# Performance work log

Hardware: AMD Instinct MI355X
Metric: run time of the kernel (lower is better)

The kernel has to match this reference:

```python
import jax, jax.numpy as jnp
import numpy as np

N_VAR = 524288   # code.n
DV = 3           # regular variable-node degree
DC = 6           # regular check-node degree
N_CHK = N_VAR * DV // DC
T = 10           # max_iterations


def setup_inputs() -> dict:
    key = jax.random.key(0)
    k1, k2, k3 = jax.random.split(key, 3)
    rng = np.random.default_rng(0)
    # Regular (3,6) Tanner graph via random socket permutation (edge list == H sparsity)
    edge_var = np.repeat(np.arange(N_VAR, dtype=np.int32), DV)
    edge_chk = rng.permutation(np.repeat(np.arange(N_CHK, dtype=np.int32), DC)).astype(np.int32)
    llr = jax.random.normal(k1, (N_VAR,), jnp.float32) * 2.0
    beta = jax.random.normal(k2, (T,), jnp.float32) * 0.1   # per-iteration dc-shared offsets
    alpha = jax.random.normal(k3, (T,), jnp.float32) * 0.1  # per-iteration dv-shared offsets
    return {"llr": llr, "beta": beta, "alpha": alpha,
            "edge_var": jnp.asarray(edge_var), "edge_chk": jnp.asarray(edge_chk),
            "n_checks": N_CHK}


def reference(llr, beta, alpha, edge_var, edge_chk, n_checks):
    E = edge_var.shape[0]
    n = llr.shape[0]
    e_idx = jnp.arange(E)

    def step(carry, ba):
        v2c, _ = carry
        b, a = ba
        mags = jnp.abs(v2c)
        sgn = jnp.sign(v2c)
        # per-check min / argmin(first) / second-min over incoming edge magnitudes
        min1 = jax.ops.segment_min(mags, edge_chk, num_segments=n_checks)
        amin = jax.ops.segment_min(jnp.where(mags == min1[edge_chk], e_idx, E),
                                   edge_chk, num_segments=n_checks)
        is_amin = e_idx == amin[edge_chk]
        min2 = jax.ops.segment_min(jnp.where(is_amin, jnp.inf, mags),
                                   edge_chk, num_segments=n_checks)
        min2 = jnp.where(jnp.isinf(min2), min1, min2)  # degree-1 checks: min2 = min1
        raw = jnp.where(is_amin, min2[edge_chk], min1[edge_chk])
        # product of signs excluding self (signs are +-1)
        sprod = jax.ops.segment_prod(sgn, edge_chk, num_segments=n_checks)
        c2v = sprod[edge_chk] * sgn * (jax.nn.relu(raw - b) - a)
        # variable node: extrinsic sum
        tot = jax.ops.segment_sum(c2v, edge_var, num_segments=n)
        v2c_new = llr[edge_var] + tot[edge_var] - c2v
        return (v2c_new, c2v), None

    v2c0 = llr[edge_var]
    (v2c_f, c2v_f), _ = jax.lax.scan(step, (v2c0, jnp.zeros_like(v2c0)), (beta, alpha))
    posterior = llr + jax.ops.segment_sum(c2v_f, edge_var, num_segments=n)
    decoded_bits = (posterior < 0).astype(jnp.int32)
    return decoded_bits, posterior
```

## Files before the change

kernel.cpp:

```cpp
#include <hip/hip_runtime.h>
#include <math.h>

#define DC_C 6
#define NRANGE 8
#define BCH 2048

__global__ __launch_bounds__(256) void build_a(const int4* __restrict__ edge_chk4,
                                               int* __restrict__ cnt,
                                               int4* __restrict__ pos4,
                                               int E4) {
    int t = blockIdx.x * blockDim.x + threadIdx.x;
    if (t >= E4) return;
    int4 c = edge_chk4[t];
    int j0 = atomicAdd(&cnt[c.x], 1);
    int j1 = atomicAdd(&cnt[c.y], 1);
    int j2 = atomicAdd(&cnt[c.z], 1);
    int j3 = atomicAdd(&cnt[c.w], 1);
    pos4[t] = make_int4(c.x * DC_C + j0, c.y * DC_C + j1,
                        c.z * DC_C + j2, c.w * DC_C + j3);
}

__global__ __launch_bounds__(256) void build_b(const int4* __restrict__ pos4,
                                               int* __restrict__ idx,
                                               int E) {
    int r = blockIdx.x & (NRANGE - 1);
    int chunk = blockIdx.x >> 3;
    int lo = r * (E / NRANGE);
    int hi = lo + (E / NRANGE);
    int base4 = chunk * (BCH / 4);
    int lim4 = E / 4;
#pragma unroll
    for (int rr = 0; rr < 2; ++rr) {
        int t4 = base4 + rr * 256 + threadIdx.x;
        if (t4 >= lim4) break;
        int4 p = pos4[t4];
        int e = t4 * 4;
        if (p.x >= lo && p.x < hi) idx[p.x] = e;
        if (p.y >= lo && p.y < hi) idx[p.y] = e + 1;
        if (p.z >= lo && p.z < hi) idx[p.z] = e + 2;
        if (p.w >= lo && p.w < hi) idx[p.w] = e + 3;
    }
}

__global__ __launch_bounds__(128, 8) void check_kernel(
        const float* __restrict__ src,
        const int* __restrict__ idx,
        float* __restrict__ c2v_s,
        const float* __restrict__ beta,
        const float* __restrict__ alpha,
        int t, int n_chk, int first) {
    int c = blockIdx.x * 128 + threadIdx.x;
    if (c >= n_chk) return;
    int base = c * DC_C;
    int2 i01 = *(const int2*)(idx + base);
    int2 i23 = *(const int2*)(idx + base + 2);
    int2 i45 = *(const int2*)(idx + base + 4);
    int e[DC_C] = {i01.x, i01.y, i23.x, i23.y, i45.x, i45.y};
    float v[DC_C];
    if (first) {
#pragma unroll
        for (int j = 0; j < DC_C; ++j) v[j] = src[e[j] / 3];
    } else {
#pragma unroll
        for (int j = 0; j < DC_C; ++j) v[j] = src[e[j]];
    }
    float b = beta[t];
    float a = alpha[t];
    float sg[DC_C], mg[DC_C];
    float sprod = 1.0f;
    float m1 = INFINITY, m2 = INFINITY;
#pragma unroll
    for (int j = 0; j < DC_C; ++j) {
        float x = v[j];
        float s = (x > 0.0f) ? 1.0f : ((x < 0.0f) ? -1.0f : 0.0f);
        float m = fabsf(x);
        sg[j] = s;
        mg[j] = m;
        sprod *= s;
        if (m < m1) { m2 = m1; m1 = m; }
        else if (m < m2) { m2 = m; }
    }
    float o[DC_C];
#pragma unroll
    for (int j = 0; j < DC_C; ++j) {
        float raw = (mg[j] == m1) ? m2 : m1;
        float val = fmaxf(raw - b, 0.0f) - a;
        o[j] = sprod * sg[j] * val;
    }
    *(float2*)(c2v_s + base)     = make_float2(o[0], o[1]);
    *(float2*)(c2v_s + base + 2) = make_float2(o[2], o[3]);
    *(float2*)(c2v_s + base + 4) = make_float2(o[4], o[5]);
}

__global__ __launch_bounds__(128, 8) void var_kernel(
        const float* __restrict__ c2v_s,
        const int* __restrict__ pos,
        const float* __restrict__ llr,
        float* __restrict__ v2c_e,
        int n) {
    int v = blockIdx.x * 128 + threadIdx.x;
    if (v >= n) return;
    int p0 = pos[v * 3 + 0];
    int p1 = pos[v * 3 + 1];
    int p2 = pos[v * 3 + 2];
    float c0 = c2v_s[p0];
    float c1 = c2v_s[p1];
    float c2 = c2v_s[p2];
    float tot = (c0 + c1) + c2;
    float t = llr[v] + tot;
    v2c_e[v * 3 + 0] = t - c0;
    v2c_e[v * 3 + 1] = t - c1;
    v2c_e[v * 3 + 2] = t - c2;
}

__global__ __launch_bounds__(128, 8) void final_kernel(
        const float* __restrict__ c2v_s,
        const int* __restrict__ pos,
        const float* __restrict__ llr,
        float* __restrict__ out,
        int n) {
    int v = blockIdx.x * 128 + threadIdx.x;
    if (v >= n) return;
    int p0 = pos[v * 3 + 0];
    int p1 = pos[v * 3 + 1];
    int p2 = pos[v * 3 + 2];
    float c0 = c2v_s[p0];
    float c1 = c2v_s[p1];
    float c2 = c2v_s[p2];
    float post = llr[v] + ((c0 + c1) + c2);
    out[v] = (post < 0.0f) ? 1.0f : 0.0f;
    out[n + v] = post;
}

extern "C" void kernel_launch(void* const* d_in, const int* in_sizes, int n_in,
                              void* d_out, int out_size, void* d_ws, size_t ws_size,
                              hipStream_t stream) {
    const float* llr      = (const float*)d_in[0];
    const float* beta     = (const float*)d_in[1];
    const float* alpha    = (const float*)d_in[2];
    const int*   edge_chk = (const int*)d_in[4];

    const int n  = in_sizes[0];
    const int T  = in_sizes[1];
    const int E  = in_sizes[3];
    const int n_chk = E / DC_C;

    char* ws = (char*)d_ws;
    int*   cnt   = (int*)ws;
    int*   pos   = (int*)(ws + (size_t)n_chk * 4);
    int*   idx   = pos + E;
    float* v2c_e = (float*)(idx + E);
    float* c2v_s = v2c_e + E;

    hipMemsetAsync(cnt, 0, (size_t)n_chk * 4, stream);
    {
        int E4 = E / 4;
        build_a<<<(E4 + 255) / 256, 256, 0, stream>>>((const int4*)edge_chk,
                                                      cnt, (int4*)pos, E4);
    }
    {
        int chunks = (E + BCH - 1) / BCH;
        build_b<<<chunks * NRANGE, 256, 0, stream>>>((const int4*)pos, idx, E);
    }
    for (int t = 0; t < T; ++t) {
        const float* src = (t == 0) ? llr : v2c_e;
        check_kernel<<<(n_chk + 127) / 128, 128, 0, stream>>>(
            src, idx, c2v_s, beta, alpha, t, n_chk, (t == 0) ? 1 : 0);
        if (t + 1 < T) {
            var_kernel<<<(n + 127) / 128, 128, 0, stream>>>(c2v_s, pos, llr,
                                                            v2c_e, n);
        } else {
            final_kernel<<<(n + 127) / 128, 128, 0, stream>>>(c2v_s, pos, llr,
                                                              (float*)d_out, n);
        }
    }
}
```

Measured before the change: 451.0 us.

## Store per-variable posterior and recompute extrinsic v2c in check kernel

The variable kernel now writes one posterior value per variable instead of three extrinsic edge messages. The check kernel rebuilds each v2c as posterior minus its own previous c2v, using a variable-index map built at setup and a zeroed c2v buffer for the first iteration. This cuts variable-kernel writes by a factor of three and makes the check-side gathers hit a smaller array with better cache locality. In exchange the check kernel reads its old c2v values, and block size moves from 128 to 256 with the launch bounds removed.

```diff
diff --git a/kernel.cpp b/kernel.cpp
--- a/kernel.cpp
+++ b/kernel.cpp
@@ -5,10 +5,10 @@
 #define NRANGE 8
 #define BCH 2048
 
-__global__ __launch_bounds__(256) void build_a(const int4* __restrict__ edge_chk4,
-                                               int* __restrict__ cnt,
-                                               int4* __restrict__ pos4,
-                                               int E4) {
+__global__ void build_a(const int4* __restrict__ edge_chk4,
+                        int* __restrict__ cnt,
+                        int4* __restrict__ pos4,
+                        int E4) {
     int t = blockIdx.x * blockDim.x + threadIdx.x;
     if (t >= E4) return;
     int4 c = edge_chk4[t];
@@ -20,9 +20,9 @@
                         c.z * DC_C + j2, c.w * DC_C + j3);
 }
 
-__global__ __launch_bounds__(256) void build_b(const int4* __restrict__ pos4,
-                                               int* __restrict__ idx,
-                                               int E) {
+__global__ void build_b(const int4* __restrict__ pos4,
+                        int* __restrict__ vmap,
+                        int E) {
     int r = blockIdx.x & (NRANGE - 1);
     int chunk = blockIdx.x >> 3;
     int lo = r * (E / NRANGE);
@@ -35,35 +35,33 @@
         if (t4 >= lim4) break;
         int4 p = pos4[t4];
         int e = t4 * 4;
-        if (p.x >= lo && p.x < hi) idx[p.x] = e;
-        if (p.y >= lo && p.y < hi) idx[p.y] = e + 1;
-        if (p.z >= lo && p.z < hi) idx[p.z] = e + 2;
-        if (p.w >= lo && p.w < hi) idx[p.w] = e + 3;
+        if (p.x >= lo && p.x < hi) vmap[p.x] = e / 3;
+        if (p.y >= lo && p.y < hi) vmap[p.y] = (e + 1) / 3;
+        if (p.z >= lo && p.z < hi) vmap[p.z] = (e + 2) / 3;
+        if (p.w >= lo && p.w < hi) vmap[p.w] = (e + 3) / 3;
     }
 }
 
-__global__ __launch_bounds__(128, 8) void check_kernel(
-        const float* __restrict__ src,
-        const int* __restrict__ idx,
-        float* __restrict__ c2v_s,
-        const float* __restrict__ beta,
-        const float* __restrict__ alpha,
-        int t, int n_chk, int first) {
-    int c = blockIdx.x * 128 + threadIdx.x;
+__global__ void check_kernel(const float* __restrict__ p,
+                             const int* __restrict__ vmap,
+                             float* __restrict__ c2v_s,
+                             const float* __restrict__ beta,
+                             const float* __restrict__ alpha,
+                             int t, int n_chk) {
+    int c = blockIdx.x * blockDim.x + threadIdx.x;
     if (c >= n_chk) return;
     int base = c * DC_C;
-    int2 i01 = *(const int2*)(idx + base);
-    int2 i23 = *(const int2*)(idx + base + 2);
-    int2 i45 = *(const int2*)(idx + base + 4);
-    int e[DC_C] = {i01.x, i01.y, i23.x, i23.y, i45.x, i45.y};
-    float v[DC_C];
-    if (first) {
+    int2 w01 = *(const int2*)(vmap + base);
+    int2 w23 = *(const int2*)(vmap + base + 2);
+    int2 w45 = *(const int2*)(vmap + base + 4);
+    float2 o01 = *(const float2*)(c2v_s + base);
+    float2 o23 = *(const float2*)(c2v_s + base + 2);
+    float2 o45 = *(const float2*)(c2v_s + base + 4);
+    int   w[DC_C]   = {w01.x, w01.y, w23.x, w23.y, w45.x, w45.y};
+    float old_[DC_C] = {o01.x, o01.y, o23.x, o23.y, o45.x, o45.y};
+    float pv[DC_C];
 #pragma unroll
-        for (int j = 0; j < DC_C; ++j) v[j] = src[e[j] / 3];
-    } else {
-#pragma unroll
-        for (int j = 0; j < DC_C; ++j) v[j] = src[e[j]];
-    }
+    for (int j = 0; j < DC_C; ++j) pv[j] = p[w[j]];
     float b = beta[t];
     float a = alpha[t];
     float sg[DC_C], mg[DC_C];
@@ -71,7 +69,7 @@
     float m1 = INFINITY, m2 = INFINITY;
 #pragma unroll
     for (int j = 0; j < DC_C; ++j) {
-        float x = v[j];
+        float x = pv[j] - old_[j];
         float s = (x > 0.0f) ? 1.0f : ((x < 0.0f) ? -1.0f : 0.0f);
         float m = fabsf(x);
         sg[j] = s;
@@ -92,13 +90,12 @@
     *(float2*)(c2v_s + base + 4) = make_float2(o[4], o[5]);
 }
 
-__global__ __launch_bounds__(128, 8) void var_kernel(
-        const float* __restrict__ c2v_s,
-        const int* __restrict__ pos,
-        const float* __restrict__ llr,
-        float* __restrict__ v2c_e,
-        int n) {
-    int v = blockIdx.x * 128 + threadIdx.x;
+__global__ void var_kernel(const float* __restrict__ c2v_s,
+                           const int* __restrict__ pos,
+                           const float* __restrict__ llr,
+                           float* __restrict__ p,
+                           int n) {
+    int v = blockIdx.x * blockDim.x + threadIdx.x;
     if (v >= n) return;
     int p0 = pos[v * 3 + 0];
     int p1 = pos[v * 3 + 1];
@@ -106,20 +103,15 @@
     float c0 = c2v_s[p0];
     float c1 = c2v_s[p1];
     float c2 = c2v_s[p2];
-    float tot = (c0 + c1) + c2;
-    float t = llr[v] + tot;
-    v2c_e[v * 3 + 0] = t - c0;
-    v2c_e[v * 3 + 1] = t - c1;
-    v2c_e[v * 3 + 2] = t - c2;
+    p[v] = llr[v] + ((c0 + c1) + c2);
 }
 
-__global__ __launch_bounds__(128, 8) void final_kernel(
-        const float* __restrict__ c2v_s,
-        const int* __restrict__ pos,
-        const float* __restrict__ llr,
-        float* __restrict__ out,
-        int n) {
-    int v = blockIdx.x * 128 + threadIdx.x;
+__global__ void final_kernel(const float* __restrict__ c2v_s,
+                             const int* __restrict__ pos,
+                             const float* __restrict__ llr,
+                             float* __restrict__ out,
+                             int n) {
+    int v = blockIdx.x * blockDim.x + threadIdx.x;
     if (v >= n) return;
     int p0 = pos[v * 3 + 0];
     int p1 = pos[v * 3 + 1];
@@ -148,11 +140,12 @@
     char* ws = (char*)d_ws;
     int*   cnt   = (int*)ws;
     int*   pos   = (int*)(ws + (size_t)n_chk * 4);
-    int*   idx   = pos + E;
-    float* v2c_e = (float*)(idx + E);
-    float* c2v_s = v2c_e + E;
+    int*   vmap  = pos + E;
+    float* c2v_s = (float*)(vmap + E);
+    float* p     = c2v_s + E;
 
     hipMemsetAsync(cnt, 0, (size_t)n_chk * 4, stream);
+    hipMemsetAsync(c2v_s, 0, (size_t)E * 4, stream);
     {
         int E4 = E / 4;
         build_a<<<(E4 + 255) / 256, 256, 0, stream>>>((const int4*)edge_chk,
@@ -160,17 +153,16 @@
     }
     {
         int chunks = (E + BCH - 1) / BCH;
-        build_b<<<chunks * NRANGE, 256, 0, stream>>>((const int4*)pos, idx, E);
+        build_b<<<chunks * NRANGE, 256, 0, stream>>>((const int4*)pos, vmap, E);
     }
     for (int t = 0; t < T; ++t) {
-        const float* src = (t == 0) ? llr : v2c_e;
-        check_kernel<<<(n_chk + 127) / 128, 128, 0, stream>>>(
-            src, idx, c2v_s, beta, alpha, t, n_chk, (t == 0) ? 1 : 0);
+        const float* src = (t == 0) ? llr : p;
+        check_kernel<<<(n_chk + 255) / 256, 256, 0, stream>>>(
+            src, vmap, c2v_s, beta, alpha, t, n_chk);
         if (t + 1 < T) {
-            var_kernel<<<(n + 127) / 128, 128, 0, stream>>>(c2v_s, pos, llr,
-                                                            v2c_e, n);
+            var_kernel<<<(n + 255) / 256, 256, 0, stream>>>(c2v_s, pos, llr, p, n);
         } else {
-            final_kernel<<<(n + 127) / 128, 128, 0, stream>>>(c2v_s, pos, llr,
+            final_kernel<<<(n + 255) / 256, 256, 0, stream>>>(c2v_s, pos, llr,
                                                               (float*)d_out, n);
         }
     }
```

Result: faster. 411.5 us (-8.7%).
